# Kernel optimization log

Hardware: AMD Instinct MI355X
Metric: run time of the kernel (lower is better)

The kernel has to match this reference:

```python
import jax, jax.numpy as jnp
import numpy as np

B, N, DIM = 8, 1024, 768
HEADS, HEAD_DIM = 8, 96
EXPERTS, TASKS = 24, 9
SCALE = HEAD_DIM ** -0.5
SWITCHLOSS_W, ZLOSS_W = 0.1, 0.001


def setup_inputs() -> dict:
    key = jax.random.key(0)
    ks = jax.random.split(key, 6)
    x = jax.random.normal(ks[0], (B, N, DIM), jnp.float32)
    Wg = jax.random.normal(ks[1], (TASKS, DIM, EXPERTS), jnp.float32) * 0.02  # per-task gate
    W1 = jax.random.normal(ks[2], (EXPERTS, DIM, HEAD_DIM), jnp.float32) * 0.02  # experts (map)
    W2 = jax.random.normal(ks[3], (EXPERTS, HEAD_DIM, DIM), jnp.float32) * 0.02  # output_experts (reduce)
    Wkv = jax.random.normal(ks[4], (DIM, 2 * HEAD_DIM), jnp.float32) * 0.02      # shared kv proj
    b_kv = jax.random.normal(ks[5], (2 * HEAD_DIM,), jnp.float32) * 0.02
    return {"x": x, "Wg\u200b".replace("\u200b", ""): Wg, "W1": W1, "W2": W2, "Wkv": Wkv, "b_kv": b_kv, "task_bh": 3}


def reference(x, Wg, W1, W2, Wkv, b_kv, task_bh):
    # ---- TaskMoE top-k gating (eval mode: clean logits, no noise/sampling) ----
    logits = jnp.einsum('bnd,de->bne', x, Wg[task_bh])            # [B,N,E]
    probs = jax.nn.softmax(logits, axis=-1)
    top_g, top_i = jax.lax.top_k(probs, HEADS)                    # [B,N,H]
    denom = jax.lax.stop_gradient(jnp.sum(top_g, -1, keepdims=True) + 1e-6)
    gates = top_g / denom                                         # normalized top-k gates

    # ---- aux losses: switch (load-balance) + z-loss (cvloss weight is 0) ----
    me = probs.reshape(-1, EXPERTS).sum(0)
    me = me / me.sum()
    freqs = jnp.zeros((EXPERTS,), x.dtype).at[top_i.reshape(-1)].add(1.0)
    fe = freqs / freqs.sum()
    switch_loss = EXPERTS * jnp.sum(me * fe)
    z_loss = jnp.mean(jax.nn.logsumexp(logits.reshape(-1, EXPERTS), axis=-1) ** 2)
    aux_loss = SWITCHLOSS_W * switch_loss + ZLOSS_W * z_loss

    # ---- MoE map: per-head q from selected experts (dense compute + gather) ----
    all_q = jnp.einsum('bnd,edh->bneh', x, W1)                    # [B,N,E,Hd]
    q = jnp.take_along_axis(all_q, top_i[..., None], axis=2)      # [B,N,H,Hd]

    # ---- shared-KV multi-head attention ----
    kv = x @ Wkv + b_kv
    k, v = jnp.split(kv, 2, axis=-1)                              # [B,N,Hd] each
    attn = jnp.einsum('bihd,bjd->bhij', q, k) * SCALE             # [B,H,N,N]
    attn = jax.nn.softmax(attn, axis=-1)
    o = jnp.einsum('bhij,bjd->bihd', attn, v)                     # [B,N,H,Hd]

    # ---- MoE reduce: gate-weighted combine through output experts ----
    comb = jax.nn.one_hot(top_i, EXPERTS, dtype=x.dtype) * gates[..., None]  # [B,N,H,E]
    mixed = jnp.einsum('bnhe,bnhd->bned', comb, o)                # [B,N,E,Hd]
    out = jnp.einsum('bned,edc->bnc', mixed, W2)                  # [B,N,DIM]
    return out, aux_loss
```

## Files before the change

### kernel.cpp

```cpp
#include <hip/hip_runtime.h>
#include <hip/hip_bf16.h>
#include <stdint.h>

#define DEVFN static __device__ __forceinline__

typedef __attribute__((ext_vector_type(8))) short bf16x8;
typedef __attribute__((ext_vector_type(4))) short s16x4;
typedef __attribute__((ext_vector_type(4))) float f32x4;

static constexpr int TOK = 8192;
static constexpr int DIM = 768;
static constexpr int HEADS = 8;
static constexpr int HD = 96;
static constexpr int EXPERTS = 24;
static constexpr int NQ = 2304;
static constexpr int NQP = 2560;
static constexpr float C2 = 0.14724484f;
static constexpr float THRRAW = 78.0f;

static constexpr size_t OFF_XB   = 0;
static constexpr size_t OFF_BT1  = 12582912;
static constexpr size_t OFF_W2T  = 16515072;
static constexpr size_t OFF_K    = 20054016;
static constexpr size_t OFF_VT   = 21626880;
static constexpr size_t OFF_GATE = 23199744;
static constexpr size_t OFF_TOPI = 23461888;
static constexpr size_t OFF_AUX  = 23724032;
static constexpr size_t OFF_ALLQ = 23724288;

DEVFN short f2bf(float f){
  __hip_bfloat16 h = __float2bfloat16(f);
  return __builtin_bit_cast(short, h);
}
DEVFN float bf2f(short u){
  return __bfloat162float(__builtin_bit_cast(__hip_bfloat16, u));
}

DEVFN void gload16(const void* g, void* l){
  auto gp = reinterpret_cast<__attribute__((address_space(1))) unsigned int*>(
      reinterpret_cast<uintptr_t>(g));
  auto lp = reinterpret_cast<__attribute__((address_space(3))) unsigned int*>(
      reinterpret_cast<uintptr_t>(l));
  __builtin_amdgcn_global_load_lds(gp, lp, 16, 0, 0);
}

__global__ __launch_bounds__(256) void prep_kernel(const float* __restrict__ x,
                                                   const float* __restrict__ W1,
                                                   const float* __restrict__ Wkv,
                                                   const float* __restrict__ W2,
                                                   short* __restrict__ xb,
                                                   short* __restrict__ Bt1,
                                                   short* __restrict__ W2t){
  int bid = blockIdx.x, tid = threadIdx.x;
  if (bid < 6144){
    int i = bid*256 + tid;
    float4 v = ((const float4*)x)[i];
    s16x4 o4;
    o4[0] = f2bf(v.x); o4[1] = f2bf(v.y); o4[2] = f2bf(v.z); o4[3] = f2bf(v.w);
    *reinterpret_cast<s16x4*>(xb + (size_t)i*4) = o4;
  } else if (bid < 13056){
    int i = (bid-6144)*256 + tid;
    int e = i / (DIM*HD);
    int rem = i - e*(DIM*HD);
    int d = rem / HD, hh = rem - d*HD;
    Bt1[(size_t)(e*HD + hh)*DIM + d] = f2bf(W1[i]);
  } else if (bid < 13632){
    int i = (bid-13056)*256 + tid;
    int d = i / 192, j = i - d*192;
    Bt1[(size_t)(NQ + j)*DIM + d] = f2bf(Wkv[i]);
  } else if (bid < 13824){
    int i = (bid-13632)*256 + tid;
    Bt1[(size_t)(NQ + 192)*DIM + i] = 0;
  } else {
    int i = (bid-13824)*256 + tid;
    int e = i / (HD*DIM);
    int rem = i - e*(HD*DIM);
    int hh = rem / DIM, c = rem - hh*DIM;
    W2t[(size_t)c*NQ + e*HD + hh] = f2bf(W2[i]);
  }
}

__global__ __launch_bounds__(256) void gating_kernel(const float* __restrict__ x,
                                                     const float* __restrict__ Wg,
                                                     const int* __restrict__ task,
                                                     int* __restrict__ topi,
                                                     float* __restrict__ gates,
                                                     float* __restrict__ auxbuf){
  __shared__ float Wl[384*25];
  __shared__ float part[16][25];
  __shared__ float lme[EXPERTS];
  __shared__ float lfr[EXPERTS];
  __shared__ float lz;
  int tid = threadIdx.x;
  int lane = tid & 63, w = tid >> 6;
  int g = lane >> 4, j = lane & 15;
  if (tid < EXPERTS){ lme[tid] = 0.f; lfr[tid] = 0.f; }
  if (tid == 0) lz = 0.f;

  int tokloc = w*4 + g;
  int token = blockIdx.x*16 + tokloc;
  const float* Wt = Wg + (size_t)task[0]*(DIM*EXPERTS);
  const float* xr = x + (size_t)token*DIM;

  float acc[EXPERTS];
#pragma unroll
  for (int e = 0; e < EXPERTS; ++e) acc[e] = 0.f;

  for (int kh = 0; kh < 2; ++kh){
    __syncthreads();
    for (int idx = tid; idx < 384*6; idx += 256){
      int d = idx / 6, q = idx - d*6;
      float4 w4 = *reinterpret_cast<const float4*>(Wt + (size_t)(kh*384 + d)*EXPERTS + q*4);
      float* dst = &Wl[d*25 + q*4];
      dst[0] = w4.x; dst[1] = w4.y; dst[2] = w4.z; dst[3] = w4.w;
    }
    __syncthreads();

#pragma unroll 2
    for (int i = 0; i < 12; ++i){
      int d = i*32 + j*2;
      float2 xv = *reinterpret_cast<const float2*>(xr + kh*384 + d);
      const float* w0 = &Wl[d*25];
#pragma unroll
      for (int e = 0; e < EXPERTS; ++e)
        acc[e] = fmaf(xv.x, w0[e], fmaf(xv.y, w0[25 + e], acc[e]));
    }

    if (kh == 0){
#pragma unroll
      for (int e = 0; e < EXPERTS; ++e){
        float v = acc[e];
#pragma unroll
        for (int m = 1; m < 16; m <<= 1) v += __shfl_xor(v, m, 64);
        acc[e] = v;
      }
      part[tokloc][j] = acc[j];
      if (j < 8) part[tokloc][16 + j] = acc[16 + j];
#pragma unroll
      for (int e = 0; e < EXPERTS; ++e) acc[e] = 0.f;
    }
  }
#pragma unroll
  for (int e = 0; e < EXPERTS; ++e){
    float v = acc[e];
#pragma unroll
    for (int m = 1; m < 16; m <<= 1) v += __shfl_xor(v, m, 64);
    acc[e] = v + part[tokloc][e];
  }

  float mx = acc[0];
#pragma unroll
  for (int e = 1; e < EXPERTS; ++e) mx = fmaxf(mx, acc[e]);
  unsigned selm = 0; int sel[8]; float sg[8];
#pragma unroll
  for (int t = 0; t < 8; ++t){
    float best = -3.0e38f; int bi = 0;
#pragma unroll
    for (int e = 0; e < EXPERTS; ++e){
      bool ok = !((selm>>e)&1u) && (acc[e] > best);
      best = ok ? acc[e] : best;
      bi   = ok ? e      : bi;
    }
    selm |= (1u<<bi); sel[t] = bi; sg[t] = best;
  }

  float S = 0.f;
#pragma unroll
  for (int e = 0; e < EXPERTS; ++e) S += __expf(acc[e] - mx);
  float lse = mx + __logf(S);
  float Sinv = 1.f/S;
  float gsum = 0.f;
#pragma unroll
  for (int t = 0; t < 8; ++t){ sg[t] = __expf(sg[t] - mx)*Sinv; gsum += sg[t]; }
  float dinv = 1.f/(gsum + 1e-6f);

  if (j == 0){
#pragma unroll
    for (int t = 0; t < 8; ++t){
      topi[token*HEADS + t]  = sel[t];
      gates[token*HEADS + t] = sg[t]*dinv;
    }
#pragma unroll
    for (int e = 0; e < EXPERTS; ++e) atomicAdd(&lme[e], __expf(acc[e] - mx)*Sinv);
#pragma unroll
    for (int t = 0; t < 8; ++t) atomicAdd(&lfr[sel[t]], 1.f);
    atomicAdd(&lz, lse*lse);
  }
  __syncthreads();
  if (tid < EXPERTS) atomicAdd(&auxbuf[tid], lme[tid]);
  else if (tid >= 32 && tid < 32+EXPERTS) atomicAdd(&auxbuf[EXPERTS + tid-32], lfr[tid-32]);
  else if (tid == 63) atomicAdd(&auxbuf[2*EXPERTS], lz);
}

__global__ void aux_final(const float* __restrict__ auxbuf, float* __restrict__ outa){
  if (threadIdx.x != 0 || blockIdx.x != 0) return;
  float ms = 0.f, fs = 0.f;
  for (int e=0;e<EXPERTS;++e){ ms += auxbuf[e]; fs += auxbuf[EXPERTS+e]; }
  float sw = 0.f;
  for (int e=0;e<EXPERTS;++e) sw += (auxbuf[e]/ms)*(auxbuf[EXPERTS+e]/fs);
  sw *= (float)EXPERTS;
  float z = auxbuf[2*EXPERTS] / (float)TOK;
  outa[0] = 0.1f*sw + 0.001f*z;
}

template<bool OUT_BF16>
__global__ __launch_bounds__(256) void gemm_bt(const short* __restrict__ A,
                                               const short* __restrict__ Bt,
                                               void* __restrict__ Cout,
                                               int M, int N, int K){
  __shared__ short As[128*64];
  __shared__ short Bs[128*64];
  int nwg = gridDim.x*gridDim.y;
  int orig = blockIdx.y*gridDim.x + blockIdx.x;
  int cpx = nwg >> 3;
  int swz = (orig & 7)*cpx + (orig >> 3);
  int bx = swz % gridDim.x, by = swz / gridDim.x;

  int tid = threadIdx.x;
  int lane = tid & 63, w = tid >> 6;
  int wr = w >> 1, wc = w & 1;
  int l15 = lane & 15, lg = lane >> 4;
  int m0 = by * 128, n0 = bx * 128;

  f32x4 acc[4][4] = {};

  for (int k0 = 0; k0 < K; k0 += 64){
#pragma unroll
    for (int it = 0; it < 4; ++it){
      int c = it*256 + tid;
      int row = c >> 3, cc = c & 7;
      int csrc = cc ^ (row & 7);
      gload16(A  + (size_t)(m0+row)*K + k0 + csrc*8, (char*)As + (size_t)c*16);
      gload16(Bt + (size_t)(n0+row)*K + k0 + csrc*8, (char*)Bs + (size_t)c*16);
    }
    __syncthreads();
#pragma unroll
    for (int kk = 0; kk < 2; ++kk){
      bf16x8 af[4], bfr[4];
      int jp = (kk*4 + lg) ^ (l15 & 7);
#pragma unroll
      for (int m = 0; m < 4; ++m)
        af[m] = *reinterpret_cast<const bf16x8*>(&As[(wr*64 + m*16 + l15)*64 + jp*8]);
#pragma unroll
      for (int n = 0; n < 4; ++n)
        bfr[n] = *reinterpret_cast<const bf16x8*>(&Bs[(wc*64 + n*16 + l15)*64 + jp*8]);
#pragma unroll
      for (int m = 0; m < 4; ++m)
#pragma unroll
        for (int n = 0; n < 4; ++n)
          acc[m][n] = __builtin_amdgcn_mfma_f32_16x16x32_bf16(af[m], bfr[n], acc[m][n], 0, 0, 0);
    }
    __syncthreads();
  }
#pragma unroll
  for (int m = 0; m < 4; ++m)
#pragma unroll
    for (int n = 0; n < 4; ++n){
      int rbase = m0 + wr*64 + m*16 + lg*4;
      int col   = n0 + wc*64 + n*16 + l15;
#pragma unroll
      for (int r = 0; r < 4; ++r){
        float v = acc[m][n][r];
        size_t idx = (size_t)(rbase + r)*N + col;
        if constexpr (OUT_BF16) ((short*)Cout)[idx] = f2bf(v);
        else                    ((float*)Cout)[idx] = v;
      }
    }
}

__global__ __launch_bounds__(256) void gemm2_fused(const short* __restrict__ o,
                                                   const int* __restrict__ topi,
                                                   const short* __restrict__ W2t,
                                                   float* __restrict__ out){
  __shared__ short As[2][128*64];
  __shared__ short Bs[2][64*64];
  __shared__ signed char hmap[128][24];
  int nwg = gridDim.x*gridDim.y;
  int orig = blockIdx.y*gridDim.x + blockIdx.x;
  int cpx = nwg >> 3;
  int swz = (orig & 7)*cpx + (orig >> 3);
  int bx = swz % gridDim.x, by = swz / gridDim.x;

  int tid = threadIdx.x;
  int lane = tid & 63, w = tid >> 6;
  int l15 = lane & 15, lg = lane >> 4;
  int m0 = by * 128, n0 = bx * 64;

  int* hm32 = (int*)&hmap[0][0];
  for (int i = tid; i < 768; i += 256) hm32[i] = -1;
  __syncthreads();
  for (int i = tid; i < 128*8; i += 256){
    int row = i >> 3, hh = i & 7;
    int e = topi[(size_t)(m0+row)*HEADS + hh];
    hmap[row][e] = (signed char)hh;
  }
  __syncthreads();

  int arow[4], accv[4];
  size_t arbase[4];
#pragma unroll
  for (int it = 0; it < 4; ++it){
    int c = it*256 + tid;
    arow[it] = c >> 3; accv[it] = c & 7;
    arbase[it] = (size_t)(m0 + arow[it])*DIM;
  }

  f32x4 acc[2][4] = {};
  bf16x8 areg[4];

#define STAGE_A(kt, dst)                                                     \
  {                                                                          \
    _Pragma("unroll")                                                        \
    for (int it = 0; it < 4; ++it){                                          \
      unsigned kc = (unsigned)((kt)*8 + accv[it]);                           \
      unsigned e = kc / 12u;                                                 \
      unsigned dc = kc - e*12u;                                              \
      int hh = hmap[arow[it]][e];                                            \
      bf16x8 av = {};                                                        \
      if (hh >= 0)                                                           \
        av = *reinterpret_cast<const bf16x8*>(o + arbase[it] + hh*HD + dc*8);\
      dst[it] = av;                                                          \
    }                                                                        \
  }
#define WRITE_A(buf, src)                                                    \
  {                                                                          \
    _Pragma("unroll")                                                        \
    for (int it = 0; it < 4; ++it)                                           \
      *reinterpret_cast<bf16x8*>(                                            \
        &As[buf][arow[it]*64 + ((accv[it] ^ (arow[it] & 7)))*8]) = src[it];  \
  }
#define STAGE_B(kt, buf)                                                     \
  {                                                                          \
    _Pragma("unroll")                                                        \
    for (int it = 0; it < 2; ++it){                                          \
      int c = it*256 + tid;                                                  \
      int row = c >> 3, cc = c & 7;                                          \
      int csrc = cc ^ (row & 7);                                             \
      gload16(W2t + (size_t)(n0+row)*NQ + (kt)*64 + csrc*8,                  \
              (char*)&Bs[buf][0] + (size_t)c*16);                            \
    }                                                                        \
  }

  STAGE_A(0, areg);
  STAGE_B(0, 0);
  WRITE_A(0, areg);
  __syncthreads();

  for (int kt = 0; kt < 36; ++kt){
    int buf = kt & 1;
    bf16x8 anext[4];
    if (kt < 35){
      STAGE_A(kt+1, anext);
      STAGE_B(kt+1, buf^1);
    }
#pragma unroll
    for (int kk = 0; kk < 2; ++kk){
      int jp = (kk*4 + lg) ^ (l15 & 7);
      bf16x8 af[2], bfr[4];
#pragma unroll
      for (int m = 0; m < 2; ++m)
        af[m] = *reinterpret_cast<const bf16x8*>(&As[buf][(w*32 + m*16 + l15)*64 + jp*8]);
#pragma unroll
      for (int n = 0; n < 4; ++n)
        bfr[n] = *reinterpret_cast<const bf16x8*>(&Bs[buf][(n*16 + l15)*64 + jp*8]);
#pragma unroll
      for (int m = 0; m < 2; ++m)
#pragma unroll
        for (int n = 0; n < 4; ++n)
          acc[m][n] = __builtin_amdgcn_mfma_f32_16x16x32_bf16(af[m], bfr[n], acc[m][n], 0, 0, 0);
    }
    if (kt < 35) WRITE_A(buf^1, anext);
    __syncthreads();
  }
#undef STAGE_A
#undef WRITE_A
#undef STAGE_B

#pragma unroll
  for (int m = 0; m < 2; ++m)
#pragma unroll
    for (int n = 0; n < 4; ++n){
      int rbase = m0 + w*32 + m*16 + lg*4;
      int col   = n0 + n*16 + l15;
#pragma unroll
      for (int r = 0; r < 4; ++r)
        out[(size_t)(rbase + r)*DIM + col] = acc[m][n][r];
    }
}

__global__ __launch_bounds__(256) void split_kv_tile(const short* __restrict__ allq,
                                                     const float* __restrict__ bkv,
                                                     short* __restrict__ Kp,
                                                     short* __restrict__ Vp){
  __shared__ short kv[64*192];
  int bt = blockIdx.x;
  int b = bt >> 4;
  int tid = threadIdx.x;
#pragma unroll
  for (int it = 0; it < 6; ++it){
    int c = it*256 + tid;
    int j = c / 24, cc = c - j*24;
    int token = b*1024 + (bt & 15)*64 + j;
    gload16(allq + (size_t)token*NQP + NQ + cc*8, (char*)kv + (size_t)c*16);
  }
  __syncthreads();
#pragma unroll
  for (int it = 0; it < 3; ++it){
    int c = it*256 + tid;
    int kc = c >> 6, j = c & 63;
    bf16x8 v = *reinterpret_cast<const bf16x8*>(&kv[j*192 + kc*8]);
    bf16x8 o8;
#pragma unroll
    for (int e = 0; e < 8; ++e) o8[e] = f2bf(bf2f(v[e]) + bkv[kc*8 + e]);
    *reinterpret_cast<bf16x8*>(Kp + ((size_t)bt*768 + c)*8) = o8;
  }
#pragma unroll
  for (int it = 0; it < 3; ++it){
    int c = it*256 + tid;
    int kc = c / 96, hd = c - kc*96;
    float bias = bkv[96 + hd];
    bf16x8 o8;
#pragma unroll
    for (int e = 0; e < 8; ++e) o8[e] = f2bf(bf2f(kv[(kc*8 + e)*192 + 96 + hd]) + bias);
    *reinterpret_cast<bf16x8*>(Vp + ((size_t)bt*768 + c)*8) = o8;
  }
}

__global__ __launch_bounds__(256, 2) void attn_fwd(const short* __restrict__ allq,
                                                   const int* __restrict__ topi,
                                                   const float* __restrict__ gates,
                                                   const short* __restrict__ Kp,
                                                   const short* __restrict__ Vp,
                                                   short* __restrict__ o){
  __shared__ short Klds[2][768*8];
  __shared__ short Vlds[2][768*8];
  __shared__ short Plds[4][16*72];
  int qt = blockIdx.x, bh = blockIdx.y;
  int b = bh >> 3, h = bh & 7;
  int tid = threadIdx.x;
  int lane = tid & 63, w = tid >> 6;
  int l15 = lane & 15, lg = lane >> 4;

  bf16x8 qf[2][3];
  int tok0 = b*1024 + qt*128 + w*32;
#pragma unroll
  for (int qm = 0; qm < 2; ++qm){
    int token = tok0 + qm*16 + l15;
    int qe = topi[token*HEADS + h];
    const short* qp = allq + (size_t)token*NQP + qe*HD;
#pragma unroll
    for (int t = 0; t < 3; ++t)
      qf[qm][t] = *reinterpret_cast<const bf16x8*>(qp + t*32 + lg*8);
  }

  f32x4 Oacc[2][6] = {};
  float mrun[2][4], lrun[2][4];
#pragma unroll
  for (int qm = 0; qm < 2; ++qm)
#pragma unroll
    for (int r = 0; r < 4; ++r){ mrun[qm][r] = -1.0e30f; lrun[qm][r] = 0.f; }

  const short* kb = Kp + (size_t)b*16*768*8;
  const short* vb = Vp + (size_t)b*16*768*8;

#pragma unroll
  for (int it = 0; it < 3; ++it){
    int c = it*256 + tid;
    gload16(kb + (size_t)c*8, (char*)&Klds[0][0] + (size_t)c*16);
    gload16(vb + (size_t)c*8, (char*)&Vlds[0][0] + (size_t)c*16);
  }
  __syncthreads();

  int cur = 0;
  for (int nt = 0; nt < 16; ++nt){
    if (nt < 15){
      const short* kn = kb + (size_t)(nt+1)*768*8;
      const short* vn = vb + (size_t)(nt+1)*768*8;
#pragma unroll
      for (int it = 0; it < 3; ++it){
        int c = it*256 + tid;
        gload16(kn + (size_t)c*8, (char*)&Klds[cur^1][0] + (size_t)c*16);
        gload16(vn + (size_t)c*8, (char*)&Vlds[cur^1][0] + (size_t)c*16);
      }
    }

    f32x4 sa[2][4];
    __builtin_amdgcn_s_setprio(1);
#pragma unroll
    for (int ct = 0; ct < 4; ++ct){
      bf16x8 kf[3];
#pragma unroll
      for (int t = 0; t < 3; ++t)
        kf[t] = *reinterpret_cast<const bf16x8*>(&Klds[cur][((t*4+lg)*64 + ct*16 + l15)*8]);
#pragma unroll
      for (int qm = 0; qm < 2; ++qm){
        f32x4 a = {};
#pragma unroll
        for (int t = 0; t < 3; ++t)
          a = __builtin_amdgcn_mfma_f32_16x16x32_bf16(qf[qm][t], kf[t], a, 0, 0, 0);
        sa[qm][ct] = a;
      }
    }
    __builtin_amdgcn_s_setprio(0);

    float pmax[2][4];
    bool need = false;
#pragma unroll
    for (int qm = 0; qm < 2; ++qm)
#pragma unroll
      for (int r = 0; r < 4; ++r){
        pmax[qm][r] = fmaxf(fmaxf(sa[qm][0][r], sa[qm][1][r]),
                            fmaxf(sa[qm][2][r], sa[qm][3][r]));
        need = need || (pmax[qm][r] > mrun[qm][r] + THRRAW);
      }
    if (__any(need)){
#pragma unroll
      for (int qm = 0; qm < 2; ++qm)
#pragma unroll
        for (int r = 0; r < 4; ++r){
          float mx = pmax[qm][r];
#pragma unroll
          for (int d = 1; d < 16; d <<= 1) mx = fmaxf(mx, __shfl_xor(mx, d, 64));
          float mnew = fmaxf(mrun[qm][r], mx);
          float al = exp2f((mrun[qm][r] - mnew)*C2);
          lrun[qm][r] *= al;
#pragma unroll
          for (int dt = 0; dt < 6; ++dt) Oacc[qm][dt][r] *= al;
          mrun[qm][r] = mnew;
        }
    }

#pragma unroll
    for (int qm = 0; qm < 2; ++qm)
#pragma unroll
      for (int r = 0; r < 4; ++r){
        float mc = mrun[qm][r]*C2;
        float s = 0.f;
#pragma unroll
        for (int ct = 0; ct < 4; ++ct){
          float p = exp2f(fmaf(sa[qm][ct][r], C2, -mc));
          sa[qm][ct][r] = p; s += p;
        }
        lrun[qm][r] += s;
      }

    bf16x8 vf[2][6];
#pragma unroll
    for (int ct = 0; ct < 4; ++ct)
#pragma unroll
      for (int r = 0; r < 4; ++r)
        Plds[w][(lg*4 + r)*72 + ct*16 + l15] = f2bf(sa[0][ct][r]);
    __builtin_amdgcn_s_setprio(1);
#pragma unroll
    for (int ks = 0; ks < 2; ++ks){
      bf16x8 pa = *reinterpret_cast<const bf16x8*>(&Plds[w][l15*72 + ks*32 + lg*8]);
#pragma unroll
      for (int dt = 0; dt < 6; ++dt){
        vf[ks][dt] = *reinterpret_cast<const bf16x8*>(&Vlds[cur][((ks*4+lg)*96 + dt*16 + l15)*8]);
        Oacc[0][dt] = __builtin_amdgcn_mfma_f32_16x16x32_bf16(pa, vf[ks][dt], Oacc[0][dt], 0, 0, 0);
      }
    }
    __builtin_amdgcn_s_setprio(0);
#pragma unroll
    for (int ct = 0; ct < 4; ++ct)
#pragma unroll
      for (int r = 0; r < 4; ++r)
        Plds[w][(lg*4 + r)*72 + ct*16 + l15] = f2bf(sa[1][ct][r]);
    __builtin_amdgcn_s_setprio(1);
#pragma unroll
    for (int ks = 0; ks < 2; ++ks){
      bf16x8 pa = *reinterpret_cast<const bf16x8*>(&Plds[w][l15*72 + ks*32 + lg*8]);
#pragma unroll
      for (int dt = 0; dt < 6; ++dt)
        Oacc[1][dt] = __builtin_amdgcn_mfma_f32_16x16x32_bf16(pa, vf[ks][dt], Oacc[1][dt], 0, 0, 0);
    }
    __builtin_amdgcn_s_setprio(0);

    __syncthreads();
    cur ^= 1;
  }

#pragma unroll
  for (int qm = 0; qm < 2; ++qm)
#pragma unroll
    for (int r = 0; r < 4; ++r){
      float l = lrun[qm][r];
#pragma unroll
      for (int d = 1; d < 16; d <<= 1) l += __shfl_xor(l, d, 64);
      int token = tok0 + qm*16 + lg*4 + r;
      float inv = gates[token*HEADS + h] / l;
#pragma unroll
      for (int dt = 0; dt < 6; ++dt)
        o[(size_t)token*DIM + h*HD + dt*16 + l15] = f2bf(Oacc[qm][dt][r]*inv);
    }
}

extern "C" void kernel_launch(void* const* d_in, const int* in_sizes, int n_in,
                              void* d_out, int out_size, void* d_ws, size_t ws_size,
                              hipStream_t stream) {
  (void)in_sizes; (void)n_in; (void)out_size; (void)ws_size;
  const float* x    = (const float*)d_in[0];
  const float* Wg   = (const float*)d_in[1];
  const float* W1   = (const float*)d_in[2];
  const float* W2   = (const float*)d_in[3];
  const float* Wkv  = (const float*)d_in[4];
  const float* bkv  = (const float*)d_in[5];
  const int*   task = (const int*)d_in[6];

  char* ws = (char*)d_ws;
  short* xb    = (short*)(ws + OFF_XB);
  short* o     = (short*)(ws + OFF_XB);
  short* Bt1   = (short*)(ws + OFF_BT1);
  short* W2t   = (short*)(ws + OFF_W2T);
  short* Kp    = (short*)(ws + OFF_K);
  short* Vp    = (short*)(ws + OFF_VT);
  float* gates = (float*)(ws + OFF_GATE);
  int*   topi  = (int*)(ws + OFF_TOPI);
  float* aux   = (float*)(ws + OFF_AUX);
  short* allq  = (short*)(ws + OFF_ALLQ);
  float* out   = (float*)d_out;

  hipMemsetAsync(aux, 0, 256, stream);
  prep_kernel  <<<20736, 256, 0, stream>>>(x, W1, Wkv, W2, xb, Bt1, W2t);
  gating_kernel<<<TOK/16, 256, 0, stream>>>(x, Wg, task, topi, gates, aux);
  aux_final    <<<1, 64, 0, stream>>>(aux, out + (size_t)TOK*DIM);
  gemm_bt<true><<<dim3(NQP/128, TOK/128), 256, 0, stream>>>(xb, Bt1, allq, TOK, NQP, DIM);
  split_kv_tile<<<128, 256, 0, stream>>>(allq, bkv, Kp, Vp);
  attn_fwd     <<<dim3(8, 64), 256, 0, stream>>>(allq, topi, gates, Kp, Vp, o);
  gemm2_fused  <<<dim3(DIM/64, TOK/128), 256, 0, stream>>>(o, topi, W2t, out);
}
```

Measured before the change: 223.7 us.

## Fuse x bf16 conversion into split-K gating and split selection kernel

Moves the x-to-bf16 conversion out of the prep kernel and into a new split-K gating kernel, so x is read from global memory once for both the conversion and the gate logits. Gating is split into a partial-logit pass, with 1024 one-wave blocks each covering 64 tokens and 96 dims, and a selection pass that sums the partials and does top-k, softmax and the aux reductions using wave shuffles. Partial sums are written to scratch that aliases the later allq buffer. The catch is that gate weights are read straight from global memory with no LDS staging, and the partial logits make an extra round trip through memory.

```diff
diff --git a/kernel.cpp b/kernel.cpp
--- a/kernel.cpp
+++ b/kernel.cpp
@@ -27,6 +27,7 @@
 static constexpr size_t OFF_TOPI = 23461888;
 static constexpr size_t OFF_AUX  = 23724032;
 static constexpr size_t OFF_ALLQ = 23724288;
+static constexpr size_t OFF_PART = OFF_ALLQ;
 
 DEVFN short f2bf(float f){
   __hip_bfloat16 h = __float2bfloat16(f);
@@ -44,35 +45,27 @@
   __builtin_amdgcn_global_load_lds(gp, lp, 16, 0, 0);
 }
 
-__global__ __launch_bounds__(256) void prep_kernel(const float* __restrict__ x,
-                                                   const float* __restrict__ W1,
+__global__ __launch_bounds__(256) void prep_kernel(const float* __restrict__ W1,
                                                    const float* __restrict__ Wkv,
                                                    const float* __restrict__ W2,
-                                                   short* __restrict__ xb,
                                                    short* __restrict__ Bt1,
                                                    short* __restrict__ W2t){
   int bid = blockIdx.x, tid = threadIdx.x;
-  if (bid < 6144){
+  if (bid < 6912){
     int i = bid*256 + tid;
-    float4 v = ((const float4*)x)[i];
-    s16x4 o4;
-    o4[0] = f2bf(v.x); o4[1] = f2bf(v.y); o4[2] = f2bf(v.z); o4[3] = f2bf(v.w);
-    *reinterpret_cast<s16x4*>(xb + (size_t)i*4) = o4;
-  } else if (bid < 13056){
-    int i = (bid-6144)*256 + tid;
     int e = i / (DIM*HD);
     int rem = i - e*(DIM*HD);
     int d = rem / HD, hh = rem - d*HD;
     Bt1[(size_t)(e*HD + hh)*DIM + d] = f2bf(W1[i]);
-  } else if (bid < 13632){
-    int i = (bid-13056)*256 + tid;
+  } else if (bid < 7488){
+    int i = (bid-6912)*256 + tid;
     int d = i / 192, j = i - d*192;
     Bt1[(size_t)(NQ + j)*DIM + d] = f2bf(Wkv[i]);
-  } else if (bid < 13824){
-    int i = (bid-13632)*256 + tid;
+  } else if (bid < 7680){
+    int i = (bid-7488)*256 + tid;
     Bt1[(size_t)(NQ + 192)*DIM + i] = 0;
   } else {
-    int i = (bid-13824)*256 + tid;
+    int i = (bid-7680)*256 + tid;
     int e = i / (HD*DIM);
     int rem = i - e*(HD*DIM);
     int hh = rem / DIM, c = rem - hh*DIM;
@@ -80,73 +73,63 @@
   }
 }
 
-__global__ __launch_bounds__(256) void gating_kernel(const float* __restrict__ x,
+__global__ __launch_bounds__(64) void gating_partial(const float* __restrict__ x,
                                                      const float* __restrict__ Wg,
                                                      const int* __restrict__ task,
-                                                     int* __restrict__ topi,
-                                                     float* __restrict__ gates,
-                                                     float* __restrict__ auxbuf){
-  __shared__ float Wl[384*25];
-  __shared__ float part[16][25];
-  __shared__ float lme[EXPERTS];
+                                                     short* __restrict__ xb,
+                                                     float* __restrict__ partial){
+  __shared__ float xl[64*101];
+  int lane = threadIdx.x;
+  int tg = blockIdx.x >> 3, kc = blockIdx.x & 7;
+  int tok0 = tg*64, kbase = kc*96;
+  const float* Wt = Wg + (size_t)task[0]*(DIM*EXPERTS) + (size_t)kbase*EXPERTS;
+
+#pragma unroll
+  for (int i = 0; i < 24; ++i){
+    int c = i*64 + lane;
+    int t = c / 24, cc = c - t*24;
+    size_t gidx = (size_t)(tok0+t)*DIM + kbase + cc*4;
+    float4 v = *reinterpret_cast<const float4*>(x + gidx);
+    float* dst = &xl[t*101 + cc*4];
+    dst[0] = v.x; dst[1] = v.y; dst[2] = v.z; dst[3] = v.w;
+    s16x4 o4;
+    o4[0] = f2bf(v.x); o4[1] = f2bf(v.y); o4[2] = f2bf(v.z); o4[3] = f2bf(v.w);
+    *reinterpret_cast<s16x4*>(xb + gidx) = o4;
+  }
+  __syncthreads();
+
+  float acc[EXPERTS];
+#pragma unroll
+  for (int e = 0; e < EXPERTS; ++e) acc[e] = 0.f;
+  for (int d = 0; d < 96; ++d){
+    float xv = xl[lane*101 + d];
+    const float* wr = Wt + d*EXPERTS;
+#pragma unroll
+    for (int e = 0; e < EXPERTS; ++e) acc[e] = fmaf(xv, wr[e], acc[e]);
+  }
+#pragma unroll
+  for (int e = 0; e < EXPERTS; ++e)
+    partial[(size_t)(kc*EXPERTS + e)*TOK + tok0 + lane] = acc[e];
+}
+
+__global__ __launch_bounds__(64) void gating_select(const float* __restrict__ partial,
+                                                    int* __restrict__ topi,
+                                                    float* __restrict__ gates,
+                                                    float* __restrict__ auxbuf){
   __shared__ float lfr[EXPERTS];
-  __shared__ float lz;
-  int tid = threadIdx.x;
-  int lane = tid & 63, w = tid >> 6;
-  int g = lane >> 4, j = lane & 15;
-  if (tid < EXPERTS){ lme[tid] = 0.f; lfr[tid] = 0.f; }
-  if (tid == 0) lz = 0.f;
-
-  int tokloc = w*4 + g;
-  int token = blockIdx.x*16 + tokloc;
-  const float* Wt = Wg + (size_t)task[0]*(DIM*EXPERTS);
-  const float* xr = x + (size_t)token*DIM;
+  int lane = threadIdx.x;
+  int token = blockIdx.x*64 + lane;
+  if (lane < EXPERTS) lfr[lane] = 0.f;
+  __syncthreads();
 
   float acc[EXPERTS];
 #pragma unroll
   for (int e = 0; e < EXPERTS; ++e) acc[e] = 0.f;
-
-  for (int kh = 0; kh < 2; ++kh){
-    __syncthreads();
-    for (int idx = tid; idx < 384*6; idx += 256){
-      int d = idx / 6, q = idx - d*6;
-      float4 w4 = *reinterpret_cast<const float4*>(Wt + (size_t)(kh*384 + d)*EXPERTS + q*4);
-      float* dst = &Wl[d*25 + q*4];
-      dst[0] = w4.x; dst[1] = w4.y; dst[2] = w4.z; dst[3] = w4.w;
-    }
-    __syncthreads();
-
-#pragma unroll 2
-    for (int i = 0; i < 12; ++i){
-      int d = i*32 + j*2;
-      float2 xv = *reinterpret_cast<const float2*>(xr + kh*384 + d);
-      const float* w0 = &Wl[d*25];
-#pragma unroll
-      for (int e = 0; e < EXPERTS; ++e)
-        acc[e] = fmaf(xv.x, w0[e], fmaf(xv.y, w0[25 + e], acc[e]));
-    }
-
-    if (kh == 0){
-#pragma unroll
-      for (int e = 0; e < EXPERTS; ++e){
-        float v = acc[e];
-#pragma unroll
-        for (int m = 1; m < 16; m <<= 1) v += __shfl_xor(v, m, 64);
-        acc[e] = v;
-      }
-      part[tokloc][j] = acc[j];
-      if (j < 8) part[tokloc][16 + j] = acc[16 + j];
-#pragma unroll
-      for (int e = 0; e < EXPERTS; ++e) acc[e] = 0.f;
-    }
-  }
-#pragma unroll
-  for (int e = 0; e < EXPERTS; ++e){
-    float v = acc[e];
-#pragma unroll
-    for (int m = 1; m < 16; m <<= 1) v += __shfl_xor(v, m, 64);
-    acc[e] = v + part[tokloc][e];
-  }
+#pragma unroll
+  for (int kc = 0; kc < 8; ++kc)
+#pragma unroll
+    for (int e = 0; e < EXPERTS; ++e)
+      acc[e] += partial[(size_t)(kc*EXPERTS + e)*TOK + token];
 
   float mx = acc[0];
 #pragma unroll
@@ -164,32 +147,37 @@
     selm |= (1u<<bi); sel[t] = bi; sg[t] = best;
   }
 
-  float S = 0.f;
-#pragma unroll
-  for (int e = 0; e < EXPERTS; ++e) S += __expf(acc[e] - mx);
+  float p[EXPERTS]; float S = 0.f;
+#pragma unroll
+  for (int e = 0; e < EXPERTS; ++e){ p[e] = __expf(acc[e] - mx); S += p[e]; }
   float lse = mx + __logf(S);
   float Sinv = 1.f/S;
-  float gsum = 0.f;
-#pragma unroll
-  for (int t = 0; t < 8; ++t){ sg[t] = __expf(sg[t] - mx)*Sinv; gsum += sg[t]; }
+  float gsum = 0.f; float pg[8];
+#pragma unroll
+  for (int t = 0; t < 8; ++t){ pg[t] = __expf(sg[t] - mx)*Sinv; gsum += pg[t]; }
   float dinv = 1.f/(gsum + 1e-6f);
 
-  if (j == 0){
-#pragma unroll
-    for (int t = 0; t < 8; ++t){
-      topi[token*HEADS + t]  = sel[t];
-      gates[token*HEADS + t] = sg[t]*dinv;
-    }
-#pragma unroll
-    for (int e = 0; e < EXPERTS; ++e) atomicAdd(&lme[e], __expf(acc[e] - mx)*Sinv);
-#pragma unroll
-    for (int t = 0; t < 8; ++t) atomicAdd(&lfr[sel[t]], 1.f);
-    atomicAdd(&lz, lse*lse);
-  }
-  __syncthreads();
-  if (tid < EXPERTS) atomicAdd(&auxbuf[tid], lme[tid]);
-  else if (tid >= 32 && tid < 32+EXPERTS) atomicAdd(&auxbuf[EXPERTS + tid-32], lfr[tid-32]);
-  else if (tid == 63) atomicAdd(&auxbuf[2*EXPERTS], lz);
+#pragma unroll
+  for (int t = 0; t < 8; ++t){
+    topi[token*HEADS + t]  = sel[t];
+    gates[token*HEADS + t] = pg[t]*dinv;
+  }
+
+  float z2 = lse*lse;
+#pragma unroll
+  for (int d = 1; d < 64; d <<= 1) z2 += __shfl_xor(z2, d, 64);
+#pragma unroll
+  for (int e = 0; e < EXPERTS; ++e){
+    float v = p[e]*Sinv;
+#pragma unroll
+    for (int d = 1; d < 64; d <<= 1) v += __shfl_xor(v, d, 64);
+    if (lane == 0) atomicAdd(&auxbuf[e], v);
+  }
+  if (lane == 0) atomicAdd(&auxbuf[2*EXPERTS], z2);
+#pragma unroll
+  for (int t = 0; t < 8; ++t) atomicAdd(&lfr[sel[t]], 1.f);
+  __syncthreads();
+  if (lane < EXPERTS) atomicAdd(&auxbuf[EXPERTS + lane], lfr[lane]);
 }
 
 __global__ void aux_final(const float* __restrict__ auxbuf, float* __restrict__ outa){
@@ -618,12 +606,14 @@
   int*   topi  = (int*)(ws + OFF_TOPI);
   float* aux   = (float*)(ws + OFF_AUX);
   short* allq  = (short*)(ws + OFF_ALLQ);
+  float* part  = (float*)(ws + OFF_PART);
   float* out   = (float*)d_out;
 
   hipMemsetAsync(aux, 0, 256, stream);
-  prep_kernel  <<<20736, 256, 0, stream>>>(x, W1, Wkv, W2, xb, Bt1, W2t);
-  gating_kernel<<<TOK/16, 256, 0, stream>>>(x, Wg, task, topi, gates, aux);
-  aux_final    <<<1, 64, 0, stream>>>(aux, out + (size_t)TOK*DIM);
+  prep_kernel   <<<14592, 256, 0, stream>>>(W1, Wkv, W2, Bt1, W2t);
+  gating_partial<<<1024, 64, 0, stream>>>(x, Wg, task, xb, part);
+  gating_select <<<128, 64, 0, stream>>>(part, topi, gates, aux);
+  aux_final     <<<1, 64, 0, stream>>>(aux, out + (size_t)TOK*DIM);
   gemm_bt<true><<<dim3(NQP/128, TOK/128), 256, 0, stream>>>(xb, Bt1, allq, TOK, NQP, DIM);
   split_kv_tile<<<128, 256, 0, stream>>>(allq, bkv, Kp, Vp);
   attn_fwd     <<<dim3(8, 64), 256, 0, stream>>>(allq, topi, gates, Kp, Vp, o);
```

Result: slower. 264.1 us (+18.1%).
